# Optimization experiments

Hardware: AMD Instinct MI355X
Metric: run time of the kernel (lower is better)

## Reference

```python
import jax, jax.numpy as jnp
import numpy as np

NU = 1.0  # degrees of freedom of the Student-t / Tsallis softmax


def setup_inputs() -> dict:
    key = jax.random.key(0)
    k1, k2, k3, k4 = jax.random.split(key, 4)
    B, Nx, Nh, Ny = 8192, 2048, 512, 1024
    x = jax.random.normal(k1, (B, Nx), dtype=jnp.float32)
    W_fc = jax.random.normal(k2, (Nh, Nx), dtype=jnp.float32) * (1.0 / np.sqrt(Nx))
    b_fc = jax.random.normal(k3, (Nh,), dtype=jnp.float32) * 0.01
    W_q = jax.random.normal(k4, (Ny, Nh), dtype=jnp.float32) * (1.0 / np.sqrt(Nh))
    return {"x": x, "W_fc": W_fc, "b_fc": b_fc, "W_q": W_q}


def reference(x, W_fc, b_fc, W_q):
    # x: [B, Nx] -> relu -> Linear(Nx, Nh) -> relu
    h = jax.nn.relu(jax.nn.relu(x) @ W_fc.T + b_fc)  # [B, Nh]
    # Quadratic layer: squared Euclidean distance to each class prototype.
    # ||h - w_j||^2 = ||h||^2 - 2 h.w_j + ||w_j||^2  (avoids [B, Ny, Nh] tensor)
    d = (jnp.sum(h * h, axis=-1, keepdims=True)
         - 2.0 * (h @ W_q.T)
         + jnp.sum(W_q * W_q, axis=-1))  # [B, Ny]
    d = jnp.maximum(d, 0.0)  # guard tiny negatives from fp cancellation
    # LogTSoftmax: p_j \propto (1 + d_j/nu)^{-(nu+1)/2}
    t = (-(NU + 1.0) / 2.0) * jnp.log1p(d / NU)  # [B, Ny]
    return t - jax.scipy.special.logsumexp(t, axis=-1, keepdims=True)
```

## Files before the change

### kernel.cpp

```cpp
#include <hip/hip_runtime.h>
#include <stdint.h>
#include <stddef.h>

#define B_ROWS 8192
#define NX 2048
#define NH 512
#define NY 1024

#define X_ELEMS (B_ROWS * NX)
#define EW_ELEMS (X_ELEMS + NH * NX)
#define EW_BLOCKS (EW_ELEMS / (8 * 256))
#define WQ_BLOCKS (NY / 4)

typedef __attribute__((ext_vector_type(8))) short bf16x8;
typedef __attribute__((ext_vector_type(4))) float f32x4;

static __device__ __forceinline__ unsigned short f2bf(float f) {
    union { float f; unsigned int u; } c; c.f = f;
    unsigned int r = 0x7FFFu + ((c.u >> 16) & 1u);
    return (unsigned short)((c.u + r) >> 16);
}

static __device__ __forceinline__ void glld16(const void* g, void* l) {
    __builtin_amdgcn_global_load_lds(
        (const __attribute__((address_space(1))) unsigned int*)g,
        (__attribute__((address_space(3))) unsigned int*)l, 16, 0, 0);
}

__global__ __launch_bounds__(256) void prep_kernel(const float* __restrict__ x,
                                                   const float* __restrict__ wfc,
                                                   const float* __restrict__ wq,
                                                   unsigned short* __restrict__ xb,
                                                   unsigned short* __restrict__ wfcb,
                                                   unsigned short* __restrict__ wqb,
                                                   float* __restrict__ wqsq,
                                                   float* __restrict__ hsq) {
    const int bid = blockIdx.x;
    const int tid = threadIdx.x;
    if (bid < EW_BLOCKS) {
        size_t idx = ((size_t)bid * 256 + tid) * 8;
        if (idx < (size_t)X_ELEMS) {
            float4 a = *(const float4*)&x[idx];
            float4 b = *(const float4*)&x[idx + 4];
            bf16x8 o;
            o[0] = (short)f2bf(fmaxf(a.x, 0.f)); o[1] = (short)f2bf(fmaxf(a.y, 0.f));
            o[2] = (short)f2bf(fmaxf(a.z, 0.f)); o[3] = (short)f2bf(fmaxf(a.w, 0.f));
            o[4] = (short)f2bf(fmaxf(b.x, 0.f)); o[5] = (short)f2bf(fmaxf(b.y, 0.f));
            o[6] = (short)f2bf(fmaxf(b.z, 0.f)); o[7] = (short)f2bf(fmaxf(b.w, 0.f));
            *(bf16x8*)&xb[idx] = o;
        } else {
            size_t off = idx - X_ELEMS;
            float4 a = *(const float4*)&wfc[off];
            float4 b = *(const float4*)&wfc[off + 4];
            bf16x8 o;
            o[0] = (short)f2bf(a.x); o[1] = (short)f2bf(a.y);
            o[2] = (short)f2bf(a.z); o[3] = (short)f2bf(a.w);
            o[4] = (short)f2bf(b.x); o[5] = (short)f2bf(b.y);
            o[6] = (short)f2bf(b.z); o[7] = (short)f2bf(b.w);
            *(bf16x8*)&wfcb[off] = o;
        }
    } else {
        const int b2 = bid - EW_BLOCKS;
        const int lane = tid & 63;
        const int row = b2 * 4 + (tid >> 6);
        const float* p = wq + (size_t)row * NH + lane * 8;
        float4 a = *(const float4*)p;
        float4 b = *(const float4*)(p + 4);
        bf16x8 o;
        o[0] = (short)f2bf(a.x); o[1] = (short)f2bf(a.y);
        o[2] = (short)f2bf(a.z); o[3] = (short)f2bf(a.w);
        o[4] = (short)f2bf(b.x); o[5] = (short)f2bf(b.y);
        o[6] = (short)f2bf(b.z); o[7] = (short)f2bf(b.w);
        *(bf16x8*)&wqb[(size_t)row * NH + lane * 8] = o;
        float s = a.x*a.x + a.y*a.y + a.z*a.z + a.w*a.w
                + b.x*b.x + b.y*b.y + b.z*b.z + b.w*b.w;
        #pragma unroll
        for (int off = 32; off > 0; off >>= 1) s += __shfl_xor(s, off);
        if (lane == 0) wqsq[row] = s;
        if (tid < 32) hsq[b2 * 32 + tid] = 0.0f;
    }
}

__global__ __launch_bounds__(512, 2) void gemm1_kernel(const unsigned short* __restrict__ xb,
                                                       const unsigned short* __restrict__ wfcb,
                                                       const float* __restrict__ b_fc,
                                                       unsigned short* __restrict__ hb,
                                                       float* __restrict__ hsq) {
    __shared__ unsigned char smem[65536];
    unsigned char* AsB = smem;
    unsigned char* BsB = smem + 32768;

    const int tid = threadIdx.x;
    const int lane = tid & 63;
    const int grp = tid >> 8;
    const int wave = (tid >> 6) & 3;
    const int wm = wave >> 1, wn = wave & 1;
    const int quad = lane >> 4;
    const int r = lane & 15;

    const int bid = blockIdx.x;
    const int n0 = ((bid >> 3) & 3) * 128;
    const int m0 = (((bid & 7) << 3) | (bid >> 5)) * 128;
    const int kbase = grp * (NX / 2);

    f32x4 acc[4][4];
    #pragma unroll
    for (int i = 0; i < 4; ++i)
        #pragma unroll
        for (int j = 0; j < 4; ++j) acc[i][j] = (f32x4)(0.0f);

    const int lrow = lane >> 2;
    const int gch = (lane & 3) ^ ((lrow >> 1) & 3);
    const char* xbB = (const char*)xb;
    const char* wfB = (const char*)wfcb;
    const int fsw = (quad ^ ((r >> 1) & 3)) * 16;

    auto stage = [&](int buf, int k0) {
        const int sb = grp * 16384 + buf * 8192;
        #pragma unroll
        for (int c = 0; c < 2; ++c) {
            int R0 = wave * 32 + c * 16;
            glld16(xbB + (size_t)(m0 + R0 + lrow) * (NX * 2) + k0 * 2 + gch * 16,
                   AsB + sb + R0 * 64);
            glld16(wfB + (size_t)(n0 + R0 + lrow) * (NX * 2) + k0 * 2 + gch * 16,
                   BsB + sb + R0 * 64);
        }
    };

    stage(0, kbase);
    #pragma unroll 1
    for (int it = 0; it < 32; ++it) {
        __syncthreads();
        if (it + 1 < 32) stage((it + 1) & 1, kbase + it * 32 + 32);
        const unsigned char* ab = AsB + grp * 16384 + (it & 1) * 8192;
        const unsigned char* bb = BsB + grp * 16384 + (it & 1) * 8192;
        bf16x8 af[4], bfv[4];
        #pragma unroll
        for (int i = 0; i < 4; ++i)
            af[i] = *(const bf16x8*)(ab + (wm * 64 + i * 16 + r) * 64 + fsw);
        #pragma unroll
        for (int j = 0; j < 4; ++j)
            bfv[j] = *(const bf16x8*)(bb + (wn * 64 + j * 16 + r) * 64 + fsw);
        #pragma unroll
        for (int i = 0; i < 4; ++i)
            #pragma unroll
            for (int j = 0; j < 4; ++j)
                acc[i][j] = __builtin_amdgcn_mfma_f32_16x16x32_bf16(af[i], bfv[j], acc[i][j], 0, 0, 0);
    }

    float* smemF = (float*)smem;
    __syncthreads();
    if (grp == 1) {
        #pragma unroll
        for (int i = 0; i < 4; ++i) {
            #pragma unroll
            for (int j = 0; j < 4; ++j) {
                int cl = wn * 64 + j * 16 + r;
                int rowb = wm * 64 + i * 16 + quad * 4;
                *(f32x4*)(smemF + cl * 128 + (rowb ^ ((cl & 7) << 2))) = acc[i][j];
            }
        }
    }
    __syncthreads();
    if (grp == 0) {
        float p[4][4];
        #pragma unroll
        for (int i = 0; i < 4; ++i)
            #pragma unroll
            for (int rr = 0; rr < 4; ++rr) p[i][rr] = 0.0f;

        #pragma unroll
        for (int i = 0; i < 4; ++i) {
            #pragma unroll
            for (int j = 0; j < 4; ++j) {
                int cl = wn * 64 + j * 16 + r;
                int rowb = wm * 64 + i * 16 + quad * 4;
                f32x4 o = *(const f32x4*)(smemF + cl * 128 + (rowb ^ ((cl & 7) << 2)));
                int col = n0 + cl;
                float bias = b_fc[col];
                #pragma unroll
                for (int rr = 0; rr < 4; ++rr) {
                    float v = fmaxf(acc[i][j][rr] + o[rr] + bias, 0.0f);
                    hb[(size_t)(m0 + rowb + rr) * NH + col] = f2bf(v);
                    p[i][rr] += v * v;
                }
            }
        }
        #pragma unroll
        for (int mask = 1; mask < 16; mask <<= 1) {
            #pragma unroll
            for (int i = 0; i < 4; ++i)
                #pragma unroll
                for (int rr = 0; rr < 4; ++rr)
                    p[i][rr] += __shfl_xor(p[i][rr], mask);
        }
        if (r == 0) {
            #pragma unroll
            for (int i = 0; i < 4; ++i)
                #pragma unroll
                for (int rr = 0; rr < 4; ++rr)
                    atomicAdd(&hsq[m0 + wm * 64 + i * 16 + quad * 4 + rr], p[i][rr]);
        }
    }
}

__global__ __launch_bounds__(1024, 4) void gemm2_kernel(const unsigned short* __restrict__ hb,
                                                        const unsigned short* __restrict__ wqb,
                                                        const float* __restrict__ hsq,
                                                        const float* __restrict__ wqsq,
                                                        float* __restrict__ out) {
    __shared__ unsigned char smem[135168];
    char* AsB = (char*)smem;
    char* BsB = (char*)smem + 4096;

    const int tid = threadIdx.x;
    const int lane = tid & 63;
    const int wave = tid >> 6;
    const int quad = lane >> 4;
    const int r = lane & 15;
    const int m0 = blockIdx.x * 32;

    f32x4 acc[2][4];
    #pragma unroll
    for (int i = 0; i < 2; ++i)
        #pragma unroll
        for (int j = 0; j < 4; ++j) acc[i][j] = (f32x4)(0.0f);

    const int lrow = lane >> 2;
    const int gch = (lane & 3) ^ ((lrow >> 1) & 3);
    const char* bsrc = (const char*)wqb + (size_t)(wave * 64 + lrow) * (NH * 2) + gch * 16;
    const char* asrc = (const char*)hb + (size_t)(m0 + wave * 16 + lrow) * (NH * 2) + gch * 16;
    const int fsw = (quad ^ ((r >> 1) & 3)) * 16;

    auto stage = [&](int buf, int k0) {
        #pragma unroll
        for (int c = 0; c < 4; ++c)
            glld16(bsrc + (size_t)k0 * 2 + c * 16 * (NH * 2),
                   BsB + buf * 65536 + (wave * 64 + c * 16) * 64);
        if (wave < 2)
            glld16(asrc + (size_t)k0 * 2, AsB + buf * 2048 + wave * 1024);
    };

    stage(0, 0);
    #pragma unroll 1
    for (int it = 0; it < NH / 32; ++it) {
        __syncthreads();
        if (it + 1 < NH / 32) stage((it + 1) & 1, it * 32 + 32);
        const char* ab = AsB + (it & 1) * 2048;
        const char* bb = BsB + (it & 1) * 65536 + wave * 4096;
        bf16x8 af[2], bfv[4];
        #pragma unroll
        for (int i = 0; i < 2; ++i)
            af[i] = *(const bf16x8*)(ab + (i * 16 + r) * 64 + fsw);
        #pragma unroll
        for (int j = 0; j < 4; ++j)
            bfv[j] = *(const bf16x8*)(bb + (j * 16 + r) * 64 + fsw);
        #pragma unroll
        for (int i = 0; i < 2; ++i)
            #pragma unroll
            for (int j = 0; j < 4; ++j)
                acc[i][j] = __builtin_amdgcn_mfma_f32_16x16x32_bf16(af[i], bfv[j], acc[i][j], 0, 0, 0);
    }

    float hs_[2][4];
    #pragma unroll
    for (int i = 0; i < 2; ++i)
        #pragma unroll
        for (int rr = 0; rr < 4; ++rr)
            hs_[i][rr] = hsq[m0 + i * 16 + quad * 4 + rr];

    float srow[2][4];
    #pragma unroll
    for (int i = 0; i < 2; ++i)
        #pragma unroll
        for (int rr = 0; rr < 4; ++rr) srow[i][rr] = 0.0f;

    #pragma unroll
    for (int j = 0; j < 4; ++j) {
        float wqv = wqsq[wave * 64 + j * 16 + r];
        #pragma unroll
        for (int i = 0; i < 2; ++i) {
            #pragma unroll
            for (int rr = 0; rr < 4; ++rr) {
                float d = hs_[i][rr] - 2.0f * acc[i][j][rr] + wqv;
                d = fmaxf(d, 0.0f);
                float onepd = 1.0f + d;
                srow[i][rr] += __builtin_amdgcn_rcpf(onepd);
                acc[i][j][rr] = -__logf(onepd);
            }
        }
    }
    #pragma unroll
    for (int mask = 1; mask < 16; mask <<= 1)
        #pragma unroll
        for (int i = 0; i < 2; ++i)
            #pragma unroll
            for (int rr = 0; rr < 4; ++rr)
                srow[i][rr] += __shfl_xor(srow[i][rr], mask);

    float* smemF = (float*)smem;
    __syncthreads();
    if (r == 0) {
        #pragma unroll
        for (int i = 0; i < 2; ++i)
            #pragma unroll
            for (int rr = 0; rr < 4; ++rr)
                smemF[wave * 32 + i * 16 + quad * 4 + rr] = srow[i][rr];
    }
    __syncthreads();
    if (tid < 32) {
        float S = 0.0f;
        #pragma unroll
        for (int w = 0; w < 16; ++w) S += smemF[w * 32 + tid];
        smemF[512 + tid] = __logf(S);
    }
    __syncthreads();

    #pragma unroll
    for (int i = 0; i < 2; ++i) {
        #pragma unroll
        for (int rr = 0; rr < 4; ++rr) {
            float l = smemF[512 + i * 16 + quad * 4 + rr];
            size_t rowoff = (size_t)(m0 + i * 16 + quad * 4 + rr) * NY + wave * 64 + r;
            #pragma unroll
            for (int j = 0; j < 4; ++j)
                out[rowoff + j * 16] = acc[i][j][rr] - l;
        }
    }
}

extern "C" void kernel_launch(void* const* d_in, const int* in_sizes, int n_in,
                              void* d_out, int out_size, void* d_ws, size_t ws_size,
                              hipStream_t stream) {
    const float* x    = (const float*)d_in[0];
    const float* W_fc = (const float*)d_in[1];
    const float* b_fc = (const float*)d_in[2];
    const float* W_q  = (const float*)d_in[3];
    float* out = (float*)d_out;

    char* ws = (char*)d_ws;
    unsigned short* xb   = (unsigned short*)(ws);
    unsigned short* wfcb = (unsigned short*)(ws + 33554432);
    unsigned short* wqb  = (unsigned short*)(ws + 35651584);
    float*          wqsq = (float*)(ws + 36700160);
    unsigned short* hb   = (unsigned short*)(ws + 36704256);
    float*          hsq  = (float*)(ws + 45092864);

    prep_kernel<<<EW_BLOCKS + WQ_BLOCKS, 256, 0, stream>>>(x, W_fc, W_q, xb, wfcb, wqb, wqsq, hsq);
    gemm1_kernel<<<256, 512, 0, stream>>>(xb, wfcb, b_fc, hb, hsq);
    gemm2_kernel<<<B_ROWS / 32, 1024, 0, stream>>>(hb, wqb, hsq, wqsq, out);
}
```

Baseline: 172.7 us.

## Fuse first GEMM into second kernel, keeping hidden activations in shared memory

Measured after the change: 195.2 us. 13.0% more time.

```diff
diff --git a/kernel.cpp b/kernel.cpp
--- a/kernel.cpp
+++ b/kernel.cpp
@@ -33,8 +33,7 @@
                                                    unsigned short* __restrict__ xb,
                                                    unsigned short* __restrict__ wfcb,
                                                    unsigned short* __restrict__ wqb,
-                                                   float* __restrict__ wqsq,
-                                                   float* __restrict__ hsq) {
+                                                   float* __restrict__ wqsq) {
     const int bid = blockIdx.x;
     const int tid = threadIdx.x;
     if (bid < EW_BLOCKS) {
@@ -77,141 +76,18 @@
         #pragma unroll
         for (int off = 32; off > 0; off >>= 1) s += __shfl_xor(s, off);
         if (lane == 0) wqsq[row] = s;
-        if (tid < 32) hsq[b2 * 32 + tid] = 0.0f;
-    }
-}
-
-__global__ __launch_bounds__(512, 2) void gemm1_kernel(const unsigned short* __restrict__ xb,
-                                                       const unsigned short* __restrict__ wfcb,
-                                                       const float* __restrict__ b_fc,
-                                                       unsigned short* __restrict__ hb,
-                                                       float* __restrict__ hsq) {
-    __shared__ unsigned char smem[65536];
-    unsigned char* AsB = smem;
-    unsigned char* BsB = smem + 32768;
-
-    const int tid = threadIdx.x;
-    const int lane = tid & 63;
-    const int grp = tid >> 8;
-    const int wave = (tid >> 6) & 3;
-    const int wm = wave >> 1, wn = wave & 1;
-    const int quad = lane >> 4;
-    const int r = lane & 15;
-
-    const int bid = blockIdx.x;
-    const int n0 = ((bid >> 3) & 3) * 128;
-    const int m0 = (((bid & 7) << 3) | (bid >> 5)) * 128;
-    const int kbase = grp * (NX / 2);
-
-    f32x4 acc[4][4];
-    #pragma unroll
-    for (int i = 0; i < 4; ++i)
-        #pragma unroll
-        for (int j = 0; j < 4; ++j) acc[i][j] = (f32x4)(0.0f);
-
-    const int lrow = lane >> 2;
-    const int gch = (lane & 3) ^ ((lrow >> 1) & 3);
-    const char* xbB = (const char*)xb;
-    const char* wfB = (const char*)wfcb;
-    const int fsw = (quad ^ ((r >> 1) & 3)) * 16;
-
-    auto stage = [&](int buf, int k0) {
-        const int sb = grp * 16384 + buf * 8192;
-        #pragma unroll
-        for (int c = 0; c < 2; ++c) {
-            int R0 = wave * 32 + c * 16;
-            glld16(xbB + (size_t)(m0 + R0 + lrow) * (NX * 2) + k0 * 2 + gch * 16,
-                   AsB + sb + R0 * 64);
-            glld16(wfB + (size_t)(n0 + R0 + lrow) * (NX * 2) + k0 * 2 + gch * 16,
-                   BsB + sb + R0 * 64);
-        }
-    };
-
-    stage(0, kbase);
-    #pragma unroll 1
-    for (int it = 0; it < 32; ++it) {
-        __syncthreads();
-        if (it + 1 < 32) stage((it + 1) & 1, kbase + it * 32 + 32);
-        const unsigned char* ab = AsB + grp * 16384 + (it & 1) * 8192;
-        const unsigned char* bb = BsB + grp * 16384 + (it & 1) * 8192;
-        bf16x8 af[4], bfv[4];
-        #pragma unroll
-        for (int i = 0; i < 4; ++i)
-            af[i] = *(const bf16x8*)(ab + (wm * 64 + i * 16 + r) * 64 + fsw);
-        #pragma unroll
-        for (int j = 0; j < 4; ++j)
-            bfv[j] = *(const bf16x8*)(bb + (wn * 64 + j * 16 + r) * 64 + fsw);
-        #pragma unroll
-        for (int i = 0; i < 4; ++i)
-            #pragma unroll
-            for (int j = 0; j < 4; ++j)
-                acc[i][j] = __builtin_amdgcn_mfma_f32_16x16x32_bf16(af[i], bfv[j], acc[i][j], 0, 0, 0);
-    }
-
-    float* smemF = (float*)smem;
-    __syncthreads();
-    if (grp == 1) {
-        #pragma unroll
-        for (int i = 0; i < 4; ++i) {
-            #pragma unroll
-            for (int j = 0; j < 4; ++j) {
-                int cl = wn * 64 + j * 16 + r;
-                int rowb = wm * 64 + i * 16 + quad * 4;
-                *(f32x4*)(smemF + cl * 128 + (rowb ^ ((cl & 7) << 2))) = acc[i][j];
-            }
-        }
-    }
-    __syncthreads();
-    if (grp == 0) {
-        float p[4][4];
-        #pragma unroll
-        for (int i = 0; i < 4; ++i)
-            #pragma unroll
-            for (int rr = 0; rr < 4; ++rr) p[i][rr] = 0.0f;
-
-        #pragma unroll
-        for (int i = 0; i < 4; ++i) {
-            #pragma unroll
-            for (int j = 0; j < 4; ++j) {
-                int cl = wn * 64 + j * 16 + r;
-                int rowb = wm * 64 + i * 16 + quad * 4;
-                f32x4 o = *(const f32x4*)(smemF + cl * 128 + (rowb ^ ((cl & 7) << 2)));
-                int col = n0 + cl;
-                float bias = b_fc[col];
-                #pragma unroll
-                for (int rr = 0; rr < 4; ++rr) {
-                    float v = fmaxf(acc[i][j][rr] + o[rr] + bias, 0.0f);
-                    hb[(size_t)(m0 + rowb + rr) * NH + col] = f2bf(v);
-                    p[i][rr] += v * v;
-                }
-            }
-        }
-        #pragma unroll
-        for (int mask = 1; mask < 16; mask <<= 1) {
-            #pragma unroll
-            for (int i = 0; i < 4; ++i)
-                #pragma unroll
-                for (int rr = 0; rr < 4; ++rr)
-                    p[i][rr] += __shfl_xor(p[i][rr], mask);
-        }
-        if (r == 0) {
-            #pragma unroll
-            for (int i = 0; i < 4; ++i)
-                #pragma unroll
-                for (int rr = 0; rr < 4; ++rr)
-                    atomicAdd(&hsq[m0 + wm * 64 + i * 16 + quad * 4 + rr], p[i][rr]);
-        }
-    }
-}
-
-__global__ __launch_bounds__(1024, 4) void gemm2_kernel(const unsigned short* __restrict__ hb,
+    }
+}
+
+__global__ __launch_bounds__(1024, 4) void fused_kernel(const unsigned short* __restrict__ xb,
+                                                        const unsigned short* __restrict__ wfcb,
                                                         const unsigned short* __restrict__ wqb,
-                                                        const float* __restrict__ hsq,
+                                                        const float* __restrict__ b_fc,
                                                         const float* __restrict__ wqsq,
                                                         float* __restrict__ out) {
-    __shared__ unsigned char smem[135168];
-    char* AsB = (char*)smem;
-    char* BsB = (char*)smem + 4096;
+    __shared__ unsigned char smem[163840];
+    char* P = (char*)smem;
+    char* H = (char*)smem + 131072;
 
     const int tid = threadIdx.x;
     const int lane = tid & 63;
@@ -220,54 +96,136 @@
     const int r = lane & 15;
     const int m0 = blockIdx.x * 32;
 
-    f32x4 acc[2][4];
-    #pragma unroll
-    for (int i = 0; i < 2; ++i)
-        #pragma unroll
-        for (int j = 0; j < 4; ++j) acc[i][j] = (f32x4)(0.0f);
-
     const int lrow = lane >> 2;
     const int gch = (lane & 3) ^ ((lrow >> 1) & 3);
-    const char* bsrc = (const char*)wqb + (size_t)(wave * 64 + lrow) * (NH * 2) + gch * 16;
-    const char* asrc = (const char*)hb + (size_t)(m0 + wave * 16 + lrow) * (NH * 2) + gch * 16;
     const int fsw = (quad ^ ((r >> 1) & 3)) * 16;
 
-    auto stage = [&](int buf, int k0) {
+    f32x4 acc1[2][2];
+    #pragma unroll
+    for (int i = 0; i < 2; ++i)
+        #pragma unroll
+        for (int j = 0; j < 2; ++j) acc1[i][j] = (f32x4)(0.0f);
+
+    const char* asrc = (const char*)xb +
+        (size_t)(m0 + (wave & 1) * 16 + lrow) * (NX * 2) + gch * 16;
+    const char* b1src = (const char*)wfcb +
+        (size_t)(wave * 32 + lrow) * (NX * 2) + gch * 16;
+
+    auto stage1 = [&](int buf, int k0) {
+        glld16(b1src + (size_t)k0 * 2, P + 4096 + buf * 32768 + (wave * 32) * 64);
+        glld16(b1src + (size_t)(16 * NX + k0) * 2, P + 4096 + buf * 32768 + (wave * 32 + 16) * 64);
+        if (wave < 2)
+            glld16(asrc + (size_t)k0 * 2, P + buf * 2048 + wave * 1024);
+    };
+
+    stage1(0, 0);
+    #pragma unroll 1
+    for (int it = 0; it < NX / 32; ++it) {
+        __syncthreads();
+        if (it + 1 < NX / 32) stage1((it + 1) & 1, it * 32 + 32);
+        const char* ab = P + (it & 1) * 2048;
+        const char* bb = P + 4096 + (it & 1) * 32768;
+        bf16x8 af[2], bfv[2];
+        #pragma unroll
+        for (int i = 0; i < 2; ++i)
+            af[i] = *(const bf16x8*)(ab + (i * 16 + r) * 64 + fsw);
+        #pragma unroll
+        for (int j = 0; j < 2; ++j)
+            bfv[j] = *(const bf16x8*)(bb + (wave * 32 + j * 16 + r) * 64 + fsw);
+        #pragma unroll
+        for (int i = 0; i < 2; ++i)
+            #pragma unroll
+            for (int j = 0; j < 2; ++j)
+                acc1[i][j] = __builtin_amdgcn_mfma_f32_16x16x32_bf16(af[i], bfv[j], acc1[i][j], 0, 0, 0);
+    }
+
+    float psum[2][4];
+    #pragma unroll
+    for (int i = 0; i < 2; ++i)
+        #pragma unroll
+        for (int rr = 0; rr < 4; ++rr) psum[i][rr] = 0.0f;
+
+    __syncthreads();
+    #pragma unroll
+    for (int j = 0; j < 2; ++j) {
+        float bias = b_fc[wave * 32 + j * 16 + r];
+        #pragma unroll
+        for (int i = 0; i < 2; ++i) {
+            #pragma unroll
+            for (int rr = 0; rr < 4; ++rr) {
+                float v = fmaxf(acc1[i][j][rr] + bias, 0.0f);
+                int row = i * 16 + quad * 4 + rr;
+                int col = wave * 32 + j * 16 + r;
+                *(unsigned short*)(H + row * 1024 + (((col >> 3) ^ (row & 7)) * 16) + (col & 7) * 2) = f2bf(v);
+                psum[i][rr] += v * v;
+            }
+        }
+    }
+    #pragma unroll
+    for (int mask = 1; mask < 16; mask <<= 1)
+        #pragma unroll
+        for (int i = 0; i < 2; ++i)
+            #pragma unroll
+            for (int rr = 0; rr < 4; ++rr)
+                psum[i][rr] += __shfl_xor(psum[i][rr], mask);
+
+    float* scr = (float*)P;
+    if (r == 0) {
+        #pragma unroll
+        for (int i = 0; i < 2; ++i)
+            #pragma unroll
+            for (int rr = 0; rr < 4; ++rr)
+                scr[wave * 32 + i * 16 + quad * 4 + rr] = psum[i][rr];
+    }
+    __syncthreads();
+    if (tid < 32) {
+        float s = 0.0f;
+        #pragma unroll
+        for (int w = 0; w < 16; ++w) s += scr[w * 32 + tid];
+        scr[512 + tid] = s;
+    }
+    __syncthreads();
+    float hs_[2][4];
+    #pragma unroll
+    for (int i = 0; i < 2; ++i)
+        #pragma unroll
+        for (int rr = 0; rr < 4; ++rr)
+            hs_[i][rr] = scr[512 + i * 16 + quad * 4 + rr];
+    __syncthreads();
+
+    f32x4 acc[2][4];
+    #pragma unroll
+    for (int i = 0; i < 2; ++i)
+        #pragma unroll
+        for (int j = 0; j < 4; ++j) acc[i][j] = (f32x4)(0.0f);
+
+    const char* b2src = (const char*)wqb + (size_t)(wave * 64 + lrow) * (NH * 2) + gch * 16;
+    auto stage2 = [&](int buf, int k0) {
         #pragma unroll
         for (int c = 0; c < 4; ++c)
-            glld16(bsrc + (size_t)k0 * 2 + c * 16 * (NH * 2),
-                   BsB + buf * 65536 + (wave * 64 + c * 16) * 64);
-        if (wave < 2)
-            glld16(asrc + (size_t)k0 * 2, AsB + buf * 2048 + wave * 1024);
+            glld16(b2src + (size_t)(c * 16 * NH + k0) * 2,
+                   P + buf * 65536 + (wave * 64 + c * 16) * 64);
     };
 
-    stage(0, 0);
+    stage2(0, 0);
     #pragma unroll 1
     for (int it = 0; it < NH / 32; ++it) {
         __syncthreads();
-        if (it + 1 < NH / 32) stage((it + 1) & 1, it * 32 + 32);
-        const char* ab = AsB + (it & 1) * 2048;
-        const char* bb = BsB + (it & 1) * 65536 + wave * 4096;
+        if (it + 1 < NH / 32) stage2((it + 1) & 1, it * 32 + 32);
+        const char* bb = P + (it & 1) * 65536;
         bf16x8 af[2], bfv[4];
         #pragma unroll
         for (int i = 0; i < 2; ++i)
-            af[i] = *(const bf16x8*)(ab + (i * 16 + r) * 64 + fsw);
+            af[i] = *(const bf16x8*)(H + (i * 16 + r) * 1024 + (((it * 4 + quad) ^ (r & 7)) * 16));
         #pragma unroll
         for (int j = 0; j < 4; ++j)
-            bfv[j] = *(const bf16x8*)(bb + (j * 16 + r) * 64 + fsw);
+            bfv[j] = *(const bf16x8*)(bb + (wave * 64 + j * 16 + r) * 64 + fsw);
         #pragma unroll
         for (int i = 0; i < 2; ++i)
             #pragma unroll
             for (int j = 0; j < 4; ++j)
                 acc[i][j] = __builtin_amdgcn_mfma_f32_16x16x32_bf16(af[i], bfv[j], acc[i][j], 0, 0, 0);
     }
-
-    float hs_[2][4];
-    #pragma unroll
-    for (int i = 0; i < 2; ++i)
-        #pragma unroll
-        for (int rr = 0; rr < 4; ++rr)
-            hs_[i][rr] = hsq[m0 + i * 16 + quad * 4 + rr];
 
     float srow[2][4];
     #pragma unroll
@@ -298,7 +256,7 @@
             for (int rr = 0; rr < 4; ++rr)
                 srow[i][rr] += __shfl_xor(srow[i][rr], mask);
 
-    float* smemF = (float*)smem;
+    float* smemF = (float*)P;
     __syncthreads();
     if (r == 0) {
         #pragma unroll
@@ -343,10 +301,7 @@
     unsigned short* wfcb = (unsigned short*)(ws + 33554432);
     unsigned short* wqb  = (unsigned short*)(ws + 35651584);
     float*          wqsq = (float*)(ws + 36700160);
-    unsigned short* hb   = (unsigned short*)(ws + 36704256);
-    float*          hsq  = (float*)(ws + 45092864);
-
-    prep_kernel<<<EW_BLOCKS + WQ_BLOCKS, 256, 0, stream>>>(x, W_fc, W_q, xb, wfcb, wqb, wqsq, hsq);
-    gemm1_kernel<<<256, 512, 0, stream>>>(xb, wfcb, b_fc, hb, hsq);
-    gemm2_kernel<<<B_ROWS / 32, 1024, 0, stream>>>(hb, wqb, hsq, wqsq, out);
-}
+
+    prep_kernel<<<EW_BLOCKS + WQ_BLOCKS, 256, 0, stream>>>(x, W_fc, W_q, xb, wfcb, wqb, wqsq);
+    fused_kernel<<<B_ROWS / 32, 1024, 0, stream>>>(xb, wfcb, wqb, b_fc, wqsq, out);
+}
```

## Triple-buffer GEMM1 loads and drop per-iteration barriers in GEMM2

Applied to the files above, without the earlier changes.

Result: faster. 162.4 us (-5.9%).

```diff
diff --git a/kernel.cpp b/kernel.cpp
--- a/kernel.cpp
+++ b/kernel.cpp
@@ -86,9 +86,9 @@
                                                        const float* __restrict__ b_fc,
                                                        unsigned short* __restrict__ hb,
                                                        float* __restrict__ hsq) {
-    __shared__ unsigned char smem[65536];
+    __shared__ unsigned char smem[98304];
     unsigned char* AsB = smem;
-    unsigned char* BsB = smem + 32768;
+    unsigned char* BsB = smem + 49152;
 
     const int tid = threadIdx.x;
     const int lane = tid & 63;
@@ -99,8 +99,9 @@
     const int r = lane & 15;
 
     const int bid = blockIdx.x;
-    const int n0 = ((bid >> 3) & 3) * 128;
-    const int m0 = (((bid & 7) << 3) | (bid >> 5)) * 128;
+    const int c_ = bid & 7, q_ = bid >> 3;
+    const int n0 = (q_ & 3) * 128;
+    const int m0 = ((c_ << 3) | (q_ >> 2)) * 128;
     const int kbase = grp * (NX / 2);
 
     f32x4 acc[4][4];
@@ -111,29 +112,39 @@
 
     const int lrow = lane >> 2;
     const int gch = (lane & 3) ^ ((lrow >> 1) & 3);
-    const char* xbB = (const char*)xb;
-    const char* wfB = (const char*)wfcb;
     const int fsw = (quad ^ ((r >> 1) & 3)) * 16;
 
-    auto stage = [&](int buf, int k0) {
-        const int sb = grp * 16384 + buf * 8192;
+    const char* asrc = (const char*)xb +
+        (size_t)(m0 + wave * 32 + lrow) * (NX * 2) + (size_t)kbase * 2 + gch * 16;
+    const char* bsrc = (const char*)wfcb +
+        (size_t)(n0 + wave * 32 + lrow) * (NX * 2) + (size_t)kbase * 2 + gch * 16;
+
+    auto stage = [&](int bi, int k0) {
+        const int sb = grp * 24576 + bi * 8192;
         #pragma unroll
         for (int c = 0; c < 2; ++c) {
-            int R0 = wave * 32 + c * 16;
-            glld16(xbB + (size_t)(m0 + R0 + lrow) * (NX * 2) + k0 * 2 + gch * 16,
-                   AsB + sb + R0 * 64);
-            glld16(wfB + (size_t)(n0 + R0 + lrow) * (NX * 2) + k0 * 2 + gch * 16,
-                   BsB + sb + R0 * 64);
+            glld16(asrc + (size_t)k0 * 2 + (size_t)c * (16 * NX * 2),
+                   AsB + sb + (wave * 32 + c * 16) * 64);
+            glld16(bsrc + (size_t)k0 * 2 + (size_t)c * (16 * NX * 2),
+                   BsB + sb + (wave * 32 + c * 16) * 64);
         }
     };
 
-    stage(0, kbase);
+    stage(0, 0);
+    stage(1, 32);
+
+    int cb = 0, sb2 = 2;
     #pragma unroll 1
     for (int it = 0; it < 32; ++it) {
-        __syncthreads();
-        if (it + 1 < 32) stage((it + 1) & 1, kbase + it * 32 + 32);
-        const unsigned char* ab = AsB + grp * 16384 + (it & 1) * 8192;
-        const unsigned char* bb = BsB + grp * 16384 + (it & 1) * 8192;
+        if (it == 31) { asm volatile("s_waitcnt vmcnt(0)" ::: "memory"); }
+        else          { asm volatile("s_waitcnt vmcnt(4)" ::: "memory"); }
+        __builtin_amdgcn_sched_barrier(0);
+        __builtin_amdgcn_s_barrier();
+        __builtin_amdgcn_sched_barrier(0);
+        if (it + 2 < 32) stage(sb2, it * 32 + 64);
+        __builtin_amdgcn_sched_barrier(0);
+        const unsigned char* ab = AsB + grp * 24576 + cb * 8192;
+        const unsigned char* bb = BsB + grp * 24576 + cb * 8192;
         bf16x8 af[4], bfv[4];
         #pragma unroll
         for (int i = 0; i < 4; ++i)
@@ -146,6 +157,8 @@
             #pragma unroll
             for (int j = 0; j < 4; ++j)
                 acc[i][j] = __builtin_amdgcn_mfma_f32_16x16x32_bf16(af[i], bfv[j], acc[i][j], 0, 0, 0);
+        cb = (cb == 2) ? 0 : cb + 1;
+        sb2 = (sb2 == 2) ? 0 : sb2 + 1;
     }
 
     float* smemF = (float*)smem;
@@ -209,9 +222,9 @@
                                                         const float* __restrict__ hsq,
                                                         const float* __restrict__ wqsq,
                                                         float* __restrict__ out) {
-    __shared__ unsigned char smem[135168];
-    char* AsB = (char*)smem;
-    char* BsB = (char*)smem + 4096;
+    __shared__ unsigned char smem[163840];
+    char* As = (char*)smem;
+    char* Bs = (char*)smem + 32768;
 
     const int tid = threadIdx.x;
     const int lane = tid & 63;
@@ -228,38 +241,50 @@
 
     const int lrow = lane >> 2;
     const int gch = (lane & 3) ^ ((lrow >> 1) & 3);
+    const int fsw = (quad ^ ((r >> 1) & 3)) * 16;
+
     const char* bsrc = (const char*)wqb + (size_t)(wave * 64 + lrow) * (NH * 2) + gch * 16;
-    const char* asrc = (const char*)hb + (size_t)(m0 + wave * 16 + lrow) * (NH * 2) + gch * 16;
-    const int fsw = (quad ^ ((r >> 1) & 3)) * 16;
-
-    auto stage = [&](int buf, int k0) {
+
+    auto stageB = [&](int buf, int k0) {
         #pragma unroll
         for (int c = 0; c < 4; ++c)
-            glld16(bsrc + (size_t)k0 * 2 + c * 16 * (NH * 2),
-                   BsB + buf * 65536 + (wave * 64 + c * 16) * 64);
-        if (wave < 2)
-            glld16(asrc + (size_t)k0 * 2, AsB + buf * 2048 + wave * 1024);
+            glld16(bsrc + (size_t)(c * 16 * NH + k0) * 2,
+                   Bs + buf * 65536 + (wave * 64 + c * 16) * 64);
     };
 
-    stage(0, 0);
+    #pragma unroll
+    for (int half = 0; half < 2; ++half)
+        glld16((const char*)hb + (size_t)(m0 + half * 16 + lrow) * (NH * 2) + wave * 64 + gch * 16,
+               As + wave * 2048 + half * 1024);
+    stageB(0, 0);
+    asm volatile("s_waitcnt vmcnt(4)" ::: "memory");
+    __builtin_amdgcn_sched_barrier(0);
+    __builtin_amdgcn_s_barrier();
+    __builtin_amdgcn_sched_barrier(0);
+
     #pragma unroll 1
     for (int it = 0; it < NH / 32; ++it) {
-        __syncthreads();
-        if (it + 1 < NH / 32) stage((it + 1) & 1, it * 32 + 32);
-        const char* ab = AsB + (it & 1) * 2048;
-        const char* bb = BsB + (it & 1) * 65536 + wave * 4096;
+        if (it + 1 < NH / 32) stageB((it + 1) & 1, it * 32 + 32);
+        __builtin_amdgcn_sched_barrier(0);
+        if (it == NH / 32 - 1) { asm volatile("s_waitcnt vmcnt(0)" ::: "memory"); }
+        else                   { asm volatile("s_waitcnt vmcnt(4)" ::: "memory"); }
+        __builtin_amdgcn_sched_barrier(0);
+        const char* ab = As + it * 2048;
+        const char* bb = Bs + (it & 1) * 65536;
         bf16x8 af[2], bfv[4];
         #pragma unroll
         for (int i = 0; i < 2; ++i)
             af[i] = *(const bf16x8*)(ab + (i * 16 + r) * 64 + fsw);
         #pragma unroll
         for (int j = 0; j < 4; ++j)
-            bfv[j] = *(const bf16x8*)(bb + (j * 16 + r) * 64 + fsw);
+            bfv[j] = *(const bf16x8*)(bb + (wave * 64 + j * 16 + r) * 64 + fsw);
+        __builtin_amdgcn_s_setprio(1);
         #pragma unroll
         for (int i = 0; i < 2; ++i)
             #pragma unroll
             for (int j = 0; j < 4; ++j)
                 acc[i][j] = __builtin_amdgcn_mfma_f32_16x16x32_bf16(af[i], bfv[j], acc[i][j], 0, 0, 0);
+        __builtin_amdgcn_s_setprio(0);
     }
 
     float hs_[2][4];
```
